# Performance work log

Hardware: AMD Instinct MI355X
Metric: run time of the kernel (lower is better)

Reference implementation:

```python
import jax, jax.numpy as jnp
import numpy as np

B, S, D, H, L, O = 64, 512, 512, 1024, 2, 1000


def setup_inputs() -> dict:
    key = jax.random.key(0)
    ks = jax.random.split(key, 12)
    s = 0.05
    return {
        "x": jax.random.normal(ks[0], (B, S, D), jnp.float32),
        "h0": jnp.zeros((L, B, H), jnp.float32),
        "c0": jnp.zeros((L, B, H), jnp.float32),
        "W_ih0": jax.random.normal(ks[1], (4 * H, D), jnp.float32) * s,
        "W_hh0": jax.random.normal(ks[2], (4 * H, H), jnp.float32) * s,
        "b_ih0": jax.random.normal(ks[3], (4 * H,), jnp.float32) * s,
        "b_hh0": jax.random.normal(ks[4], (4 * H,), jnp.float32) * s,
        "W_ih1": jax.random.normal(ks[5], (4 * H, H), jnp.float32) * s,
        "W_hh1": jax.random.normal(ks[6], (4 * H, H), jnp.float32) * s,
        "b_ih1": jax.random.normal(ks[7], (4 * H,), jnp.float32) * s,
        "b_hh1": jax.random.normal(ks[8], (4 * H,), jnp.float32) * s,
        "W_fc": jax.random.normal(ks[9], (O, H), jnp.float32) * s,
        "b_fc": jax.random.normal(ks[10], (O,), jnp.float32) * s,
    }


def _lstm_cell(x_t, h, c, W_ih, W_hh, b_ih, b_hh):
    # standard LSTMCell: fused 4-gate GEMM, gate order (i, f, g, o)
    gates = x_t @ W_ih.T + b_ih + h @ W_hh.T + b_hh  # [B, 4H]
    i, f, g, o = jnp.split(gates, 4, axis=-1)
    i = jax.nn.sigmoid(i)
    f = jax.nn.sigmoid(f)
    g = jnp.tanh(g)
    o = jax.nn.sigmoid(o)
    c_new = f * c + i * g
    h_new = o * jnp.tanh(c_new)
    return h_new, c_new


def reference(x, h0, c0, W_ih0, W_hh0, b_ih0, b_hh0, W_ih1, W_hh1, b_ih1, b_hh1, W_fc, b_fc):
    params = [(W_ih0, W_hh0, b_ih0, b_hh0), (W_ih1, W_hh1, b_ih1, b_hh1)]

    def step(carry, x_t):
        hs, cs = carry  # tuples of [B,H] per layer
        new_h, new_c = [], []
        inp = x_t
        for l in range(L):  # fixed small layer count
            h_l, c_l = _lstm_cell(inp, hs[l], cs[l], *params[l])
            new_h.append(h_l)
            new_c.append(c_l)
            inp = h_l
        return (tuple(new_h), tuple(new_c)), None

    xs = jnp.swapaxes(x, 0, 1)  # [S, B, D]
    init = (tuple(h0[l] for l in range(L)), tuple(c0[l] for l in range(L)))
    (hs, _), _ = jax.lax.scan(step, init, xs)
    # dropout is inference-mode identity; output_activation=None
    out = hs[-1] @ W_fc.T + b_fc  # [B, O]
    return out
```

## Files before the change

### kernel.cpp

```cpp
#include <hip/hip_runtime.h>

#define B_ 64
#define S_ 512
#define D_ 512
#define H_ 1024

typedef __attribute__((ext_vector_type(8))) short bf16x8;
typedef __attribute__((ext_vector_type(4))) float f32x4;
typedef unsigned short u16;
typedef unsigned int u32;

#define MFMA(a, b, c) __builtin_amdgcn_mfma_f32_16x16x32_bf16(a, b, c, 0, 0, 0)

__device__ __forceinline__ u16 f2bf(float f) {
    u32 u = __float_as_uint(f);
    u += 0x7fffu + ((u >> 16) & 1u);
    return (u16)(u >> 16);
}
__device__ __forceinline__ float sigm(float x) { return 1.0f / (1.0f + __expf(-x)); }
__device__ __forceinline__ float tanh_f(float x) { return 1.0f - 2.0f / (__expf(2.0f * x) + 1.0f); }

__device__ __forceinline__ bf16x8 cvt8(const float* p) {
    float4 f0 = ((const float4*)p)[0];
    float4 f1 = ((const float4*)p)[1];
    bf16x8 v;
    v[0] = (short)f2bf(f0.x); v[1] = (short)f2bf(f0.y);
    v[2] = (short)f2bf(f0.z); v[3] = (short)f2bf(f0.w);
    v[4] = (short)f2bf(f1.x); v[5] = (short)f2bf(f1.y);
    v[6] = (short)f2bf(f1.z); v[7] = (short)f2bf(f1.w);
    return v;
}

__device__ __forceinline__ void llc_ld(bf16x8& d, const u16* p) {
    asm volatile("global_load_dwordx4 %0, %1, off sc0 sc1" : "=v"(d) : "v"(p));
}
__device__ __forceinline__ void vm0() {
    asm volatile("s_waitcnt vmcnt(0)" ::: "memory");
}
__device__ __forceinline__ void vmw16() {
    asm volatile("s_waitcnt vmcnt(16)" ::: "memory");
}
__device__ __forceinline__ void fence_frag(bf16x8& d) {
    asm volatile("" : "+v"(d));
}
__device__ __forceinline__ void llc_st16(u16* p, u16 v) {
    u32 vv = v;
    asm volatile("global_store_short %0, %1, off sc0 sc1" :: "v"(p), "v"(vv) : "memory");
}
__device__ __forceinline__ void llc_st32(int* p, int v) {
    asm volatile("global_store_dword %0, %1, off sc0 sc1" :: "v"(p), "v"(v) : "memory");
}
__device__ __forceinline__ void llc_ld2(int& a, int& b, const int* p0, const int* p1) {
    asm volatile("global_load_dword %0, %2, off sc0 sc1\n"
                 "global_load_dword %1, %3, off sc0 sc1\n"
                 "s_waitcnt vmcnt(0)"
                 : "=&v"(a), "=&v"(b) : "v"(p0), "v"(p1) : "memory");
}

__global__ void prep_w(const float* __restrict__ Wih, const float* __restrict__ Whh,
                       u16* __restrict__ Wc, int Kx, int Kw, int total8) {
    int idx = blockIdx.x * 256 + threadIdx.x;
    if (idx >= total8) return;
    int kc8 = Kw >> 3;
    int n = idx / kc8;
    int kc = (idx - n * kc8) << 3;
    const float* src = (kc < Kx) ? (Wih + (size_t)n * Kx + kc)
                                 : (Whh + (size_t)n * (Kw - Kx) + (kc - Kx));
    *(bf16x8*)(Wc + (size_t)n * Kw + kc) = cvt8(src);
}

__global__ void prep_misc2(const float* __restrict__ h0in,
                           const float* __restrict__ bih0, const float* __restrict__ bhh0,
                           const float* __restrict__ bih1, const float* __restrict__ bhh1,
                           float* __restrict__ bias0, float* __restrict__ bias1,
                           u16* __restrict__ h0a, u16* __restrict__ h0b,
                           u16* __restrict__ h1a, u16* __restrict__ h1b,
                           int* __restrict__ bar) {
    int idx = blockIdx.x * 256 + threadIdx.x;
    if (idx < 8192) bar[idx] = 0;
    if (idx < 4096) { bias0[idx] = bih0[idx] + bhh0[idx]; return; }
    if (idx < 8192) { int i = idx - 4096; bias1[i] = bih1[i] + bhh1[i]; return; }
    int r = idx - 8192;
    if (r >= 2 * B_ * H_) return;
    int l = r >> 16;
    int rr = r & 65535;
    u16 hb = f2bf(h0in[r]);
    if (l == 0) { h0a[rr] = hb; h0b[rr] = hb; }
    else        { h1a[rr] = hb; h1b[rr] = hb; }
}

__global__ __launch_bounds__(512, 2) void lstm_persist(
    const float* __restrict__ x,
    const u16* __restrict__ W0c, const u16* __restrict__ W1c,
    const float* __restrict__ bias0, const float* __restrict__ bias1,
    const float* __restrict__ c0in,
    u16* __restrict__ h0a, u16* __restrict__ h0b,
    u16* __restrict__ h1a, u16* __restrict__ h1b,
    float* __restrict__ h1f,
    int* __restrict__ bar) {
    const int bk = blockIdx.x;
    const int cgp = bk >> 1;
    const int mh = bk & 1;
    const int tid = threadIdx.x;
    const int w = tid >> 6;
    const int lane = tid & 63;
    const int quad = lane >> 4;
    const int l16 = lane & 15;

    int gc[2];
    #pragma unroll
    for (int n = 0; n < 2; ++n) {
        int c = n * 16 + l16;
        gc[n] = (c >> 3) * 1024 + cgp * 8 + (c & 7);
    }

    bf16x8 w0x[2][2], w0h[2][4];
    bf16x8 w1f[2][8];
    #pragma unroll
    for (int n = 0; n < 2; ++n) {
        #pragma unroll
        for (int kf = 0; kf < 2; ++kf)
            w0x[n][kf] = *(const bf16x8*)(W0c + (size_t)gc[n] * 1536 + w * 64 + kf * 32 + quad * 8);
        #pragma unroll
        for (int kf = 0; kf < 4; ++kf)
            w0h[n][kf] = *(const bf16x8*)(W0c + (size_t)gc[n] * 1536 + 512 + w * 128 + kf * 32 + quad * 8);
        #pragma unroll
        for (int kf = 0; kf < 8; ++kf)
            w1f[n][kf] = *(const bf16x8*)(W1c + (size_t)gc[n] * 2048 + w * 256 + kf * 32 + quad * 8);
    }

    __shared__ __align__(16) float partA[8 * 32 * 36];
    __shared__ __align__(16) float partB[8 * 32 * 36];
    __shared__ float c0l[256], c1l[256];
    __shared__ __align__(16) float b0l[32], b1l[32];

    if (tid < 32) {
        int gg = tid >> 3, j = tid & 7;
        b0l[j * 4 + gg] = bias0[gg * 1024 + cgp * 8 + j];
        b1l[j * 4 + gg] = bias1[gg * 1024 + cgp * 8 + j];
    }
    if (tid < 256) {
        int b = tid >> 3, j = tid & 7;
        int gi = (mh * 32 + b) * 1024 + cgp * 8 + j;
        c0l[tid] = c0in[gi];
        c1l[tid] = c0in[65536 + gi];
    }
    __syncthreads();

    const int brow0 = mh * 32 + l16;
    const int brow1 = brow0 + 16;

    const int* q0 = bar + (2 * lane + mh) * 32;
    const int* q1 = bar + (2 * (lane + 64) + mh) * 32;
    const int co0 = (l16 & 7) * 4 + (l16 >> 3);
    const int co1 = co0 + 2;

    f32x4 xacc[2][2];
    #define XPART(t)                                                                 \
        {                                                                            \
            xacc[0][0] = (f32x4){0.f,0.f,0.f,0.f}; xacc[0][1] = (f32x4){0.f,0.f,0.f,0.f}; \
            xacc[1][0] = (f32x4){0.f,0.f,0.f,0.f}; xacc[1][1] = (f32x4){0.f,0.f,0.f,0.f}; \
            _Pragma("unroll")                                                        \
            for (int kf = 0; kf < 2; ++kf) {                                         \
                int k = w * 64 + kf * 32 + quad * 8;                                 \
                bf16x8 a0 = cvt8(x + (size_t)brow0 * 262144 + (t) * 512 + k);        \
                bf16x8 a1 = cvt8(x + (size_t)brow1 * 262144 + (t) * 512 + k);        \
                xacc[0][0] = MFMA(a0, w0x[0][kf], xacc[0][0]);                       \
                xacc[0][1] = MFMA(a0, w0x[1][kf], xacc[0][1]);                       \
                xacc[1][0] = MFMA(a1, w0x[0][kf], xacc[1][0]);                       \
                xacc[1][1] = MFMA(a1, w0x[1][kf], xacc[1][1]);                       \
            }                                                                        \
        }

    XPART(0);

    for (int p = 0; p <= S_; ++p) {
        const int rd = p & 1;
        const u16* h0r = rd ? h0b : h0a;
        u16*       h0w_ = rd ? h0a : h0b;
        const u16* h1r = rd ? h1b : h1a;
        u16*       h1w_ = rd ? h1a : h1b;

        if (p > 0) {
            int f0, f1;
            for (int it = 0; it < 40000; ++it) {
                llc_ld2(f0, f1, q0, q1);
                if (__all((f0 >= p) && (f1 >= p))) break;
            }
        }

        bf16x8 a0[4], a1[4], pb0[8], pb1[8];
        if (p < S_) {
            #pragma unroll
            for (int kf = 0; kf < 4; ++kf) {
                int ko = w * 128 + kf * 32 + quad * 8;
                llc_ld(a0[kf], h0r + brow0 * 1024 + ko);
                llc_ld(a1[kf], h0r + brow1 * 1024 + ko);
            }
        }
        if (p >= 1) {
            #pragma unroll
            for (int kf = 0; kf < 8; ++kf) {
                int k = w * 256 + kf * 32;
                const u16* src = (k < 1024) ? h0r : h1r;
                int ko = (k & 1023) + quad * 8;
                llc_ld(pb0[kf], src + brow0 * 1024 + ko);
                llc_ld(pb1[kf], src + brow1 * 1024 + ko);
            }
        }

        if (p < S_) {
            if (p >= 1) vmw16(); else vm0();
            #pragma unroll
            for (int kf = 0; kf < 4; ++kf) { fence_frag(a0[kf]); fence_frag(a1[kf]); }
            f32x4 acc00 = xacc[0][0], acc01 = xacc[0][1];
            f32x4 acc10 = xacc[1][0], acc11 = xacc[1][1];
            #pragma unroll
            for (int kf = 0; kf < 4; ++kf) {
                acc00 = MFMA(a0[kf], w0h[0][kf], acc00);
                acc01 = MFMA(a0[kf], w0h[1][kf], acc01);
                acc10 = MFMA(a1[kf], w0h[0][kf], acc10);
                acc11 = MFMA(a1[kf], w0h[1][kf], acc11);
            }
            #pragma unroll
            for (int r = 0; r < 4; ++r) {
                int b0 = quad * 4 + r, b1 = b0 + 16;
                partA[w * 1152 + b0 * 36 + co0] = acc00[r];
                partA[w * 1152 + b0 * 36 + co1] = acc01[r];
                partA[w * 1152 + b1 * 36 + co0] = acc10[r];
                partA[w * 1152 + b1 * 36 + co1] = acc11[r];
            }
        }
        __syncthreads();

        if (p >= 1) {
            vm0();
            #pragma unroll
            for (int kf = 0; kf < 8; ++kf) { fence_frag(pb0[kf]); fence_frag(pb1[kf]); }
        }

        if (p < S_ && tid < 256) {
            int b = tid >> 3, j = tid & 7;
            f32x4 s = *(const f32x4*)&b0l[j * 4];
            #pragma unroll
            for (int w8 = 0; w8 < 8; ++w8)
                s += *(const f32x4*)&partA[w8 * 1152 + b * 36 + j * 4];
            float c = c0l[tid];
            float cn = sigm(s[1]) * c + sigm(s[0]) * tanh_f(s[2]);
            float hn = sigm(s[3]) * tanh_f(cn);
            c0l[tid] = cn;
            llc_st16(h0w_ + (mh * 32 + b) * 1024 + cgp * 8 + j, f2bf(hn));
        }

        if (p >= 1) {
            f32x4 acc00 = {0.f,0.f,0.f,0.f}, acc01 = {0.f,0.f,0.f,0.f};
            f32x4 acc10 = {0.f,0.f,0.f,0.f}, acc11 = {0.f,0.f,0.f,0.f};
            #pragma unroll
            for (int kf = 0; kf < 8; ++kf) {
                acc00 = MFMA(pb0[kf], w1f[0][kf], acc00);
                acc01 = MFMA(pb0[kf], w1f[1][kf], acc01);
                acc10 = MFMA(pb1[kf], w1f[0][kf], acc10);
                acc11 = MFMA(pb1[kf], w1f[1][kf], acc11);
            }
            #pragma unroll
            for (int r = 0; r < 4; ++r) {
                int b0 = quad * 4 + r, b1 = b0 + 16;
                partB[w * 1152 + b0 * 36 + co0] = acc00[r];
                partB[w * 1152 + b0 * 36 + co1] = acc01[r];
                partB[w * 1152 + b1 * 36 + co0] = acc10[r];
                partB[w * 1152 + b1 * 36 + co1] = acc11[r];
            }
        }
        __syncthreads();
        if (p >= 1 && tid < 256) {
            int b = tid >> 3, j = tid & 7;
            f32x4 s = *(const f32x4*)&b1l[j * 4];
            #pragma unroll
            for (int w8 = 0; w8 < 8; ++w8)
                s += *(const f32x4*)&partB[w8 * 1152 + b * 36 + j * 4];
            float c = c1l[tid];
            float cn = sigm(s[1]) * c + sigm(s[0]) * tanh_f(s[2]);
            float hn = sigm(s[3]) * tanh_f(cn);
            c1l[tid] = cn;
            int gi = (mh * 32 + b) * 1024 + cgp * 8 + j;
            llc_st16(h1w_ + gi, f2bf(hn));
            if (p == S_) h1f[gi] = hn;
        }

        if (p < S_) {
            vm0();
            __syncthreads();
            if (tid == 0) llc_st32(bar + bk * 32, p + 1);
            if (p + 1 < S_) XPART(p + 1);
        }
    }
}

__global__ void fc_k(const float* __restrict__ h1f, const float* __restrict__ Wfc,
                     const float* __restrict__ bfc, float* __restrict__ out) {
    int idx = blockIdx.x * 256 + threadIdx.x;
    if (idx >= 64 * 1000) return;
    int o = idx % 1000;
    int b = idx / 1000;
    const float4* hr = (const float4*)(h1f + b * H_);
    const float4* wr = (const float4*)(Wfc + (size_t)o * H_);
    float s = 0.f;
    #pragma unroll 4
    for (int k = 0; k < 256; ++k) {
        float4 a = hr[k];
        float4 w = wr[k];
        s += a.x * w.x + a.y * w.y + a.z * w.z + a.w * w.w;
    }
    out[idx] = s + bfc[o];
}

extern "C" void kernel_launch(void* const* d_in, const int* in_sizes, int n_in,
                              void* d_out, int out_size, void* d_ws, size_t ws_size,
                              hipStream_t stream) {
    const float* x    = (const float*)d_in[0];
    const float* h0in = (const float*)d_in[1];
    const float* c0in = (const float*)d_in[2];
    const float* Wih0 = (const float*)d_in[3];
    const float* Whh0 = (const float*)d_in[4];
    const float* bih0 = (const float*)d_in[5];
    const float* bhh0 = (const float*)d_in[6];
    const float* Wih1 = (const float*)d_in[7];
    const float* Whh1 = (const float*)d_in[8];
    const float* bih1 = (const float*)d_in[9];
    const float* bhh1 = (const float*)d_in[10];
    const float* Wfc  = (const float*)d_in[11];
    const float* bfc  = (const float*)d_in[12];
    float* out = (float*)d_out;

    char* ws = (char*)d_ws;
    size_t off = 0;
    auto alloc = [&](size_t bytes) {
        void* p = ws + off;
        off += (bytes + 255) & ~(size_t)255;
        return p;
    };
    u16* W0c   = (u16*)alloc((size_t)4096 * 1536 * 2);
    u16* W1c   = (u16*)alloc((size_t)4096 * 2048 * 2);
    float* bias0 = (float*)alloc(4096 * 4);
    float* bias1 = (float*)alloc(4096 * 4);
    u16* h0A   = (u16*)alloc(B_ * H_ * 2);
    u16* h0B   = (u16*)alloc(B_ * H_ * 2);
    u16* h1A   = (u16*)alloc(B_ * H_ * 2);
    u16* h1B   = (u16*)alloc(B_ * H_ * 2);
    float* h1f = (float*)alloc(B_ * H_ * 4);
    int* bar   = (int*)alloc(32768);

    prep_w<<<786432 / 256, 256, 0, stream>>>(Wih0, Whh0, W0c, 512, 1536, 786432);
    prep_w<<<1048576 / 256, 256, 0, stream>>>(Wih1, Whh1, W1c, 1024, 2048, 1048576);
    prep_misc2<<<(8192 + 2 * B_ * H_ + 255) / 256, 256, 0, stream>>>(
        h0in, bih0, bhh0, bih1, bhh1, bias0, bias1, h0A, h0B, h1A, h1B, bar);

    void* args[] = {(void*)&x, (void*)&W0c, (void*)&W1c, (void*)&bias0, (void*)&bias1,
                    (void*)&c0in, (void*)&h0A, (void*)&h0B, (void*)&h1A, (void*)&h1B,
                    (void*)&h1f, (void*)&bar};
    hipLaunchCooperativeKernel((void*)lstm_persist, dim3(256), dim3(512), args, 0, stream);

    fc_k<<<(64000 + 255) / 256, 256, 0, stream>>>(h1f, Wfc, bfc, out);
}
```

Baseline: 6.250 ms.

## Replicate hidden state per XCD into pre-swizzled mirrors with hierarchical barrier

Each block reads its XCD id at startup. A few 'importer' blocks per XCD wait for all producers, then copy the bf16 h0/h1 state into a per-XCD, 4-way rotated mirror buffer already laid out in MFMA fragment order. Compute blocks then read that mirror with plain cached loads instead of LLC-bypassing loads from the global buffer, and wait on a local XCD flag rather than polling every block's flag. This aims to cut cross-XCD traffic and the cost of the all-to-all polling, but adds an extra copy stage, more barrier hops, and a larger workspace on the critical path of every timestep.

```diff
diff --git a/kernel.cpp b/kernel.cpp
--- a/kernel.cpp
+++ b/kernel.cpp
@@ -37,9 +37,6 @@
 __device__ __forceinline__ void vm0() {
     asm volatile("s_waitcnt vmcnt(0)" ::: "memory");
 }
-__device__ __forceinline__ void vmw16() {
-    asm volatile("s_waitcnt vmcnt(16)" ::: "memory");
-}
 __device__ __forceinline__ void fence_frag(bf16x8& d) {
     asm volatile("" : "+v"(d));
 }
@@ -50,11 +47,22 @@
 __device__ __forceinline__ void llc_st32(int* p, int v) {
     asm volatile("global_store_dword %0, %1, off sc0 sc1" :: "v"(p), "v"(v) : "memory");
 }
-__device__ __forceinline__ void llc_ld2(int& a, int& b, const int* p0, const int* p1) {
-    asm volatile("global_load_dword %0, %2, off sc0 sc1\n"
-                 "global_load_dword %1, %3, off sc0 sc1\n"
+__device__ __forceinline__ int llc_poll1(const int* p) {
+    int v;
+    asm volatile("global_load_dword %0, %1, off sc0 sc1\ns_waitcnt vmcnt(0)"
+                 : "=v"(v) : "v"(p) : "memory");
+    return v;
+}
+__device__ __forceinline__ void llc_ld_i4(int& v0, int& v1, int& v2, int& v3,
+                                          const int* p0, const int* p1,
+                                          const int* p2, const int* p3) {
+    asm volatile("global_load_dword %0, %4, off sc0 sc1\n"
+                 "global_load_dword %1, %5, off sc0 sc1\n"
+                 "global_load_dword %2, %6, off sc0 sc1\n"
+                 "global_load_dword %3, %7, off sc0 sc1\n"
                  "s_waitcnt vmcnt(0)"
-                 : "=&v"(a), "=&v"(b) : "v"(p0), "v"(p1) : "memory");
+                 : "=&v"(v0), "=&v"(v1), "=&v"(v2), "=&v"(v3)
+                 : "v"(p0), "v"(p1), "v"(p2), "v"(p3) : "memory");
 }
 
 __global__ void prep_w(const float* __restrict__ Wih, const float* __restrict__ Whh,
@@ -77,7 +85,7 @@
                            u16* __restrict__ h1a, u16* __restrict__ h1b,
                            int* __restrict__ bar) {
     int idx = blockIdx.x * 256 + threadIdx.x;
-    if (idx < 8192) bar[idx] = 0;
+    if (idx < 10240) bar[idx] = 0;
     if (idx < 4096) { bias0[idx] = bih0[idx] + bhh0[idx]; return; }
     if (idx < 8192) { int i = idx - 4096; bias1[i] = bih1[i] + bhh1[i]; return; }
     int r = idx - 8192;
@@ -97,7 +105,8 @@
     u16* __restrict__ h0a, u16* __restrict__ h0b,
     u16* __restrict__ h1a, u16* __restrict__ h1b,
     float* __restrict__ h1f,
-    int* __restrict__ bar) {
+    int* __restrict__ bar,
+    u16* __restrict__ mirrA, u16* __restrict__ mirrB) {
     const int bk = blockIdx.x;
     const int cgp = bk >> 1;
     const int mh = bk & 1;
@@ -106,6 +115,35 @@
     const int lane = tid & 63;
     const int quad = lane >> 4;
     const int l16 = lane & 15;
+
+    int* pflag  = bar;
+    int* regcnt = bar + 8192;
+    int* gbar   = bar + 8208;
+    int* xdone  = bar + 8216;
+
+    __shared__ int sh4[4];
+    if (tid == 0) {
+        int xc;
+        asm volatile("s_getreg_b32 %0, hwreg(HW_REG_XCC_ID, 0, 4)" : "=s"(xc));
+        xc &= 7;
+        int rk = __hip_atomic_fetch_add(&regcnt[xc], 1, __ATOMIC_RELAXED, __HIP_MEMORY_SCOPE_AGENT);
+        __hip_atomic_fetch_add(gbar, 1, __ATOMIC_RELAXED, __HIP_MEMORY_SCOPE_AGENT);
+        for (int it = 0; it < 4000000; ++it) {
+            if (__hip_atomic_load(gbar, __ATOMIC_RELAXED, __HIP_MEMORY_SCOPE_AGENT) >= 256) break;
+            __builtin_amdgcn_s_sleep(2);
+        }
+        int msk = 0;
+        for (int xx = 0; xx < 8; ++xx)
+            if (__hip_atomic_load(&regcnt[xx], __ATOMIC_RELAXED, __HIP_MEMORY_SCOPE_AGENT) > 0)
+                msk |= 1 << xx;
+        int nx = __hip_atomic_load(&regcnt[xc], __ATOMIC_RELAXED, __HIP_MEMORY_SCOPE_AGENT);
+        int im = (nx >= 8) ? 8 : (nx >= 4) ? 4 : (nx >= 2) ? 2 : 1;
+        sh4[0] = xc; sh4[1] = rk; sh4[2] = im; sh4[3] = msk;
+    }
+    __syncthreads();
+    const int xcc = sh4[0], rank = sh4[1], imp = sh4[2], xmask = sh4[3];
+    const bool isImp = rank < imp;
+    int* lflagX = bar + 8448 + xcc * 64;
 
     int gc[2];
     #pragma unroll
@@ -149,9 +187,6 @@
 
     const int brow0 = mh * 32 + l16;
     const int brow1 = brow0 + 16;
-
-    const int* q0 = bar + (2 * lane + mh) * 32;
-    const int* q1 = bar + (2 * (lane + 64) + mh) * 32;
     const int co0 = (l16 & 7) * 4 + (l16 >> 3);
     const int co1 = co0 + 2;
 
@@ -163,12 +198,12 @@
             _Pragma("unroll")                                                        \
             for (int kf = 0; kf < 2; ++kf) {                                         \
                 int k = w * 64 + kf * 32 + quad * 8;                                 \
-                bf16x8 a0 = cvt8(x + (size_t)brow0 * 262144 + (t) * 512 + k);        \
-                bf16x8 a1 = cvt8(x + (size_t)brow1 * 262144 + (t) * 512 + k);        \
-                xacc[0][0] = MFMA(a0, w0x[0][kf], xacc[0][0]);                       \
-                xacc[0][1] = MFMA(a0, w0x[1][kf], xacc[0][1]);                       \
-                xacc[1][0] = MFMA(a1, w0x[0][kf], xacc[1][0]);                       \
-                xacc[1][1] = MFMA(a1, w0x[1][kf], xacc[1][1]);                       \
+                bf16x8 a0_ = cvt8(x + (size_t)brow0 * 262144 + (t) * 512 + k);       \
+                bf16x8 a1_ = cvt8(x + (size_t)brow1 * 262144 + (t) * 512 + k);       \
+                xacc[0][0] = MFMA(a0_, w0x[0][kf], xacc[0][0]);                      \
+                xacc[0][1] = MFMA(a0_, w0x[1][kf], xacc[0][1]);                      \
+                xacc[1][0] = MFMA(a1_, w0x[0][kf], xacc[1][0]);                      \
+                xacc[1][1] = MFMA(a1_, w0x[1][kf], xacc[1][1]);                      \
             }                                                                        \
         }
 
@@ -176,43 +211,57 @@
 
     for (int p = 0; p <= S_; ++p) {
         const int rd = p & 1;
-        const u16* h0r = rd ? h0b : h0a;
-        u16*       h0w_ = rd ? h0a : h0b;
-        const u16* h1r = rd ? h1b : h1a;
-        u16*       h1w_ = rd ? h1a : h1b;
-
-        if (p > 0) {
-            int f0, f1;
-            for (int it = 0; it < 40000; ++it) {
-                llc_ld2(f0, f1, q0, q1);
-                if (__all((f0 >= p) && (f1 >= p))) break;
+        const int rot = p & 3;
+        u16* h0w_ = rd ? h0a : h0b;
+        u16* h1w_ = rd ? h1a : h1b;
+
+        if (p >= 2) {
+            const int* xp = xdone + (lane & 7);
+            const bool act = (xmask >> (lane & 7)) & 1;
+            for (int it = 0; it < 200000; ++it) {
+                int v = llc_poll1(xp);
+                if (__all(!act || v >= p - 1)) break;
+            }
+        }
+        if (p >= 1) {
+            const int* fp = lflagX + (((lane & 7) < imp) ? (lane & 7) : 0);
+            for (int it = 0; it < 400000; ++it) {
+                int v = llc_poll1(fp);
+                if (__all(v >= p)) break;
             }
         }
 
         bf16x8 a0[4], a1[4], pb0[8], pb1[8];
         if (p < S_) {
-            #pragma unroll
-            for (int kf = 0; kf < 4; ++kf) {
-                int ko = w * 128 + kf * 32 + quad * 8;
-                llc_ld(a0[kf], h0r + brow0 * 1024 + ko);
-                llc_ld(a1[kf], h0r + brow1 * 1024 + ko);
+            if (p == 0) {
+                #pragma unroll
+                for (int kf = 0; kf < 4; ++kf) {
+                    int ko = w * 128 + kf * 32 + quad * 8;
+                    llc_ld(a0[kf], h0a + brow0 * 1024 + ko);
+                    llc_ld(a1[kf], h0a + brow1 * 1024 + ko);
+                }
+                vm0();
+                #pragma unroll
+                for (int kf = 0; kf < 4; ++kf) { fence_frag(a0[kf]); fence_frag(a1[kf]); }
+            } else {
+                const u16* MAc = mirrA + (((size_t)xcc * 4 + rot) * 2 + mh) * 32768 + (size_t)tid * 64;
+                #pragma unroll
+                for (int kf = 0; kf < 4; ++kf) {
+                    a0[kf] = *(const bf16x8*)(MAc + kf * 16);
+                    a1[kf] = *(const bf16x8*)(MAc + kf * 16 + 8);
+                }
             }
         }
         if (p >= 1) {
+            const u16* MBc = mirrB + (((size_t)xcc * 4 + rot) * 2 + mh) * 65536 + (size_t)tid * 128;
             #pragma unroll
             for (int kf = 0; kf < 8; ++kf) {
-                int k = w * 256 + kf * 32;
-                const u16* src = (k < 1024) ? h0r : h1r;
-                int ko = (k & 1023) + quad * 8;
-                llc_ld(pb0[kf], src + brow0 * 1024 + ko);
-                llc_ld(pb1[kf], src + brow1 * 1024 + ko);
+                pb0[kf] = *(const bf16x8*)(MBc + kf * 16);
+                pb1[kf] = *(const bf16x8*)(MBc + kf * 16 + 8);
             }
         }
 
         if (p < S_) {
-            if (p >= 1) vmw16(); else vm0();
-            #pragma unroll
-            for (int kf = 0; kf < 4; ++kf) { fence_frag(a0[kf]); fence_frag(a1[kf]); }
             f32x4 acc00 = xacc[0][0], acc01 = xacc[0][1];
             f32x4 acc10 = xacc[1][0], acc11 = xacc[1][1];
             #pragma unroll
@@ -232,12 +281,6 @@
             }
         }
         __syncthreads();
-
-        if (p >= 1) {
-            vm0();
-            #pragma unroll
-            for (int kf = 0; kf < 8; ++kf) { fence_frag(pb0[kf]); fence_frag(pb1[kf]); }
-        }
 
         if (p < S_ && tid < 256) {
             int b = tid >> 3, j = tid & 7;
@@ -290,7 +333,165 @@
         if (p < S_) {
             vm0();
             __syncthreads();
-            if (tid == 0) llc_st32(bar + bk * 32, p + 1);
+            if (tid == 0) llc_st32(pflag + bk * 32, p + 1);
+
+            if (isImp) {
+                if (w == 0) {
+                    const int* f0 = pflag + (lane * 4 + 0) * 32;
+                    const int* f1 = pflag + (lane * 4 + 1) * 32;
+                    const int* f2 = pflag + (lane * 4 + 2) * 32;
+                    const int* f3 = pflag + (lane * 4 + 3) * 32;
+                    for (int it = 0; it < 200000; ++it) {
+                        int v0, v1, v2, v3;
+                        llc_ld_i4(v0, v1, v2, v3, f0, f1, f2, f3);
+                        int mn = v0 < v1 ? v0 : v1;
+                        int mn2 = v2 < v3 ? v2 : v3;
+                        mn = mn < mn2 ? mn : mn2;
+                        if (__all(mn >= p + 1)) break;
+                    }
+                }
+                __syncthreads();
+                const int rd2 = (p + 1) & 1;
+                const int rot2 = (p + 1) & 3;
+                const u16* H0 = rd2 ? h0b : h0a;
+                const u16* H1 = rd2 ? h1b : h1a;
+                u16* MAw = mirrA + ((size_t)xcc * 4 + rot2) * 2 * 32768;
+                u16* MBw = mirrB + ((size_t)xcc * 4 + rot2) * 2 * 65536;
+
+                if (imp == 8) {
+                    const int sub = rank & 1;
+                    const int s12 = (rank >> 1) * 512 + tid;
+                    const int hf = s12 >> 10;
+                    const int pr = s12 & 1023;
+                    const int mh2 = pr >> 9, tc = pr & 511;
+                    const int wc = tc >> 6, qc = (tc >> 4) & 3, lc = tc & 15;
+                    const size_t r0 = (size_t)(mh2 * 32 + lc) * 1024 + qc * 8;
+                    const size_t r1 = r0 + 16384;
+                    u16* dA = MAw + mh2 * 32768 + tc * 64;
+                    u16* dB = MBw + mh2 * 65536 + tc * 128;
+                    bf16x8 t0, t1, t2, t3, t4, t5;
+                    if (hf == 0) {
+                        if (sub == 0) {
+                            llc_ld(t0, H0 + r0 + wc * 128 + 0);
+                            llc_ld(t1, H0 + r1 + wc * 128 + 0);
+                            llc_ld(t2, H0 + r0 + wc * 128 + 32);
+                            llc_ld(t3, H0 + r1 + wc * 128 + 32);
+                            llc_ld(t4, H0 + r0 + wc * 128 + 64);
+                            llc_ld(t5, H0 + r1 + wc * 128 + 64);
+                            vm0();
+                            fence_frag(t0); fence_frag(t1); fence_frag(t2);
+                            fence_frag(t3); fence_frag(t4); fence_frag(t5);
+                            *(bf16x8*)(dA + 0)  = t0; *(bf16x8*)(dA + 8)  = t1;
+                            *(bf16x8*)(dA + 16) = t2; *(bf16x8*)(dA + 24) = t3;
+                            *(bf16x8*)(dA + 32) = t4; *(bf16x8*)(dA + 40) = t5;
+                        } else {
+                            llc_ld(t0, H0 + r0 + wc * 128 + 96);
+                            llc_ld(t1, H0 + r1 + wc * 128 + 96);
+                            { int k = wc * 256;      const u16* Sp = (k < 1024) ? H0 : H1;
+                              llc_ld(t2, Sp + r0 + (k & 1023)); llc_ld(t3, Sp + r1 + (k & 1023)); }
+                            { int k = wc * 256 + 32; const u16* Sp = (k < 1024) ? H0 : H1;
+                              llc_ld(t4, Sp + r0 + (k & 1023)); llc_ld(t5, Sp + r1 + (k & 1023)); }
+                            vm0();
+                            fence_frag(t0); fence_frag(t1); fence_frag(t2);
+                            fence_frag(t3); fence_frag(t4); fence_frag(t5);
+                            *(bf16x8*)(dA + 48) = t0; *(bf16x8*)(dA + 56) = t1;
+                            *(bf16x8*)(dB + 0)  = t2; *(bf16x8*)(dB + 8)  = t3;
+                            *(bf16x8*)(dB + 16) = t4; *(bf16x8*)(dB + 24) = t5;
+                        }
+                    } else {
+                        const int kfb = 2 + sub * 3;
+                        { int k = wc * 256 + (kfb + 0) * 32; const u16* Sp = (k < 1024) ? H0 : H1;
+                          llc_ld(t0, Sp + r0 + (k & 1023)); llc_ld(t1, Sp + r1 + (k & 1023)); }
+                        { int k = wc * 256 + (kfb + 1) * 32; const u16* Sp = (k < 1024) ? H0 : H1;
+                          llc_ld(t2, Sp + r0 + (k & 1023)); llc_ld(t3, Sp + r1 + (k & 1023)); }
+                        { int k = wc * 256 + (kfb + 2) * 32; const u16* Sp = (k < 1024) ? H0 : H1;
+                          llc_ld(t4, Sp + r0 + (k & 1023)); llc_ld(t5, Sp + r1 + (k & 1023)); }
+                        vm0();
+                        fence_frag(t0); fence_frag(t1); fence_frag(t2);
+                        fence_frag(t3); fence_frag(t4); fence_frag(t5);
+                        *(bf16x8*)(dB + (kfb + 0) * 16)     = t0;
+                        *(bf16x8*)(dB + (kfb + 0) * 16 + 8) = t1;
+                        *(bf16x8*)(dB + (kfb + 1) * 16)     = t2;
+                        *(bf16x8*)(dB + (kfb + 1) * 16 + 8) = t3;
+                        *(bf16x8*)(dB + (kfb + 2) * 16)     = t4;
+                        *(bf16x8*)(dB + (kfb + 2) * 16 + 8) = t5;
+                    }
+                } else {
+                    for (int s = rank * 512 + tid; s < 2048; s += imp * 512) {
+                        const int hf = s >> 10;
+                        const int pr = s & 1023;
+                        const int mh2 = pr >> 9, tc = pr & 511;
+                        const int wc = tc >> 6, qc = (tc >> 4) & 3, lc = tc & 15;
+                        const size_t r0 = (size_t)(mh2 * 32 + lc) * 1024 + qc * 8;
+                        const size_t r1 = r0 + 16384;
+                        u16* dA = MAw + mh2 * 32768 + tc * 64;
+                        u16* dB = MBw + mh2 * 65536 + tc * 128;
+                        bf16x8 t0, t1, t2, t3, t4, t5;
+                        #pragma unroll
+                        for (int g = 0; g < 2; ++g) {
+                            if (hf == 0) {
+                                if (g == 0) {
+                                    llc_ld(t0, H0 + r0 + wc * 128 + 0);
+                                    llc_ld(t1, H0 + r1 + wc * 128 + 0);
+                                    llc_ld(t2, H0 + r0 + wc * 128 + 32);
+                                    llc_ld(t3, H0 + r1 + wc * 128 + 32);
+                                    llc_ld(t4, H0 + r0 + wc * 128 + 64);
+                                    llc_ld(t5, H0 + r1 + wc * 128 + 64);
+                                } else {
+                                    llc_ld(t0, H0 + r0 + wc * 128 + 96);
+                                    llc_ld(t1, H0 + r1 + wc * 128 + 96);
+                                    { int k = wc * 256;      const u16* Sp = (k < 1024) ? H0 : H1;
+                                      llc_ld(t2, Sp + r0 + (k & 1023)); llc_ld(t3, Sp + r1 + (k & 1023)); }
+                                    { int k = wc * 256 + 32; const u16* Sp = (k < 1024) ? H0 : H1;
+                                      llc_ld(t4, Sp + r0 + (k & 1023)); llc_ld(t5, Sp + r1 + (k & 1023)); }
+                                }
+                            } else {
+                                const int kfb = 2 + g * 3;
+                                { int k = wc * 256 + (kfb + 0) * 32; const u16* Sp = (k < 1024) ? H0 : H1;
+                                  llc_ld(t0, Sp + r0 + (k & 1023)); llc_ld(t1, Sp + r1 + (k & 1023)); }
+                                { int k = wc * 256 + (kfb + 1) * 32; const u16* Sp = (k < 1024) ? H0 : H1;
+                                  llc_ld(t2, Sp + r0 + (k & 1023)); llc_ld(t3, Sp + r1 + (k & 1023)); }
+                                { int k = wc * 256 + (kfb + 2) * 32; const u16* Sp = (k < 1024) ? H0 : H1;
+                                  llc_ld(t4, Sp + r0 + (k & 1023)); llc_ld(t5, Sp + r1 + (k & 1023)); }
+                            }
+                            vm0();
+                            fence_frag(t0); fence_frag(t1); fence_frag(t2);
+                            fence_frag(t3); fence_frag(t4); fence_frag(t5);
+                            if (hf == 0) {
+                                if (g == 0) {
+                                    *(bf16x8*)(dA + 0)  = t0; *(bf16x8*)(dA + 8)  = t1;
+                                    *(bf16x8*)(dA + 16) = t2; *(bf16x8*)(dA + 24) = t3;
+                                    *(bf16x8*)(dA + 32) = t4; *(bf16x8*)(dA + 40) = t5;
+                                } else {
+                                    *(bf16x8*)(dA + 48) = t0; *(bf16x8*)(dA + 56) = t1;
+                                    *(bf16x8*)(dB + 0)  = t2; *(bf16x8*)(dB + 8)  = t3;
+                                    *(bf16x8*)(dB + 16) = t4; *(bf16x8*)(dB + 24) = t5;
+                                }
+                            } else {
+                                const int kfb = 2 + g * 3;
+                                *(bf16x8*)(dB + (kfb + 0) * 16)     = t0;
+                                *(bf16x8*)(dB + (kfb + 0) * 16 + 8) = t1;
+                                *(bf16x8*)(dB + (kfb + 1) * 16)     = t2;
+                                *(bf16x8*)(dB + (kfb + 1) * 16 + 8) = t3;
+                                *(bf16x8*)(dB + (kfb + 2) * 16)     = t4;
+                                *(bf16x8*)(dB + (kfb + 2) * 16 + 8) = t5;
+                            }
+                        }
+                    }
+                }
+                vm0();
+                __syncthreads();
+                if (tid == 0)
+                    llc_st32(lflagX + rank, p + 1);
+                if (rank == 0 && w == 0) {
+                    const int* sf = lflagX + (lane & 7);
+                    for (int it = 0; it < 300000; ++it) {
+                        int v = llc_poll1(sf);
+                        if (__all(v >= p + 1 || (lane & 7) >= imp)) break;
+                    }
+                    if (lane == 0) llc_st32(xdone + xcc, p + 1);
+                }
+            }
             if (p + 1 < S_) XPART(p + 1);
         }
     }
@@ -348,7 +549,9 @@
     u16* h1A   = (u16*)alloc(B_ * H_ * 2);
     u16* h1B   = (u16*)alloc(B_ * H_ * 2);
     float* h1f = (float*)alloc(B_ * H_ * 4);
-    int* bar   = (int*)alloc(32768);
+    int* bar   = (int*)alloc(40960);
+    u16* mirrA = (u16*)alloc((size_t)8 * 4 * 2 * 32768 * 2);
+    u16* mirrB = (u16*)alloc((size_t)8 * 4 * 2 * 65536 * 2);
 
     prep_w<<<786432 / 256, 256, 0, stream>>>(Wih0, Whh0, W0c, 512, 1536, 786432);
     prep_w<<<1048576 / 256, 256, 0, stream>>>(Wih1, Whh1, W1c, 1024, 2048, 1048576);
@@ -357,7 +560,7 @@
 
     void* args[] = {(void*)&x, (void*)&W0c, (void*)&W1c, (void*)&bias0, (void*)&bias1,
                     (void*)&c0in, (void*)&h0A, (void*)&h0B, (void*)&h1A, (void*)&h1B,
-                    (void*)&h1f, (void*)&bar};
+                    (void*)&h1f, (void*)&bar, (void*)&mirrA, (void*)&mirrB};
     hipLaunchCooperativeKernel((void*)lstm_persist, dim3(256), dim3(512), args, 0, stream);
 
     fc_k<<<(64000 + 255) / 256, 256, 0, stream>>>(h1f, Wfc, bfc, out);
```

After: 11.85 ms. +89.6%, slower.
